# Optimization experiments

Measured on AMD Instinct MI355X. Metric: run time of the kernel, lower is better.

## Reference

```python
import jax, jax.numpy as jnp
import numpy as np

DIRECTIONS = [(0, 0), (1, 0), (-1, 0), (0, 1), (0, -1)]  # (dx, dy)
BN_EPS = 1e-5


def shift2d(x, directions=DIRECTIONS):
    # x: (B, C, H, W). Split channels into G groups, roll each spatially,
    # zero out the wrapped-around border (zero_pad mode), then concat.
    C = x.shape[1]
    G = len(directions)
    base = C // G
    sizes = [base] * (G - 1) + [C - base * (G - 1)]
    starts = np.concatenate([[0], np.cumsum(sizes)])
    out = []
    for i, (dx, dy) in enumerate(directions):
        chunk = x[:, starts[i]:starts[i + 1]]
        if dx == 0 and dy == 0:
            out.append(chunk)
            continue
        y = jnp.roll(chunk, shift=(dy, dx), axis=(-2, -1))
        if dy > 0:
            y = y.at[..., :dy, :].set(0.0)
        elif dy < 0:
            y = y.at[..., dy:, :].set(0.0)
        if dx > 0:
            y = y.at[..., :, :dx].set(0.0)
        elif dx < 0:
            y = y.at[..., :, dx:].set(0.0)
        out.append(y)
    return jnp.concatenate(out, axis=1)


def setup_inputs() -> dict:
    key = jax.random.key(0)
    k1, k2, k3, k4 = jax.random.split(key, 4)
    B, Cin, Cout, H, W = 32, 256, 256, 56, 56
    x = jax.random.normal(k1, (B, Cin, H, W), dtype=jnp.float32)
    pw_w = jax.random.normal(k2, (Cout, Cin), dtype=jnp.float32) * (1.0 / np.sqrt(Cin))
    gamma = jnp.ones((Cout,), dtype=jnp.float32)
    beta = jnp.zeros((Cout,), dtype=jnp.float32)
    running_mean = jax.random.normal(k3, (Cout,), dtype=jnp.float32) * 0.1
    running_var = jax.random.uniform(k4, (Cout,), dtype=jnp.float32, minval=0.5, maxval=1.5)
    return {"x": x, "pw_w": pw_w, "gamma": gamma, "beta": beta,
            "running_mean": running_mean, "running_var": running_var}


def reference(x, pw_w, gamma, beta, running_mean, running_var):
    # Shift (parameter-free spatial mixing)
    y = shift2d(x)
    # stride=1 -> down is Identity
    # 1x1 conv (no bias): pointwise channel mixing
    y = jnp.einsum('bchw,oc->bohw', y, pw_w)
    # BatchNorm2d (inference form with running stats) + ReLU
    inv = gamma * jax.lax.rsqrt(running_var + BN_EPS)
    y = y * inv[None, :, None, None] + (beta - running_mean * inv)[None, :, None, None]
    return jax.nn.relu(y)
```

## Files before the change

### kernel.cpp

```cpp
#include <hip/hip_runtime.h>

#define H_ 56
#define W_ 56
#define HW_ 3136
#define CIN_ 256
#define COUT_ 256

typedef __attribute__((ext_vector_type(8))) short short8;
typedef __attribute__((ext_vector_type(4))) float f32x4;

__device__ unsigned short g_wbf[COUT_ * CIN_];

__device__ __forceinline__ unsigned short f2bf(float f) {
  union { float f; unsigned int i; } v; v.f = f;
  unsigned int b = v.i + (0x7fffu + ((v.i >> 16) & 1u));
  return (unsigned short)(b >> 16);
}

__device__ __forceinline__ void gload_lds16(const unsigned short* g, unsigned short* l) {
  __builtin_amdgcn_global_load_lds(
      (const __attribute__((address_space(1))) unsigned int*)g,
      (__attribute__((address_space(3))) unsigned int*)l, 16, 0, 0);
}

__global__ __launch_bounds__(256)
void prep_weights(const float* __restrict__ wgt) {
  int idx = blockIdx.x * 256 + threadIdx.x;
  int bm  = idx >> 15;
  int kt  = (idx >> 13) & 3;
  int e   = idx & 8191;
  int m   = e >> 6;
  int u   = (e >> 3) & 7;
  int j   = e & 7;
  int o   = bm * 128 + m;
  int k   = kt * 64 + (((u ^ (m & 7)) << 3) | j);
  g_wbf[idx] = f2bf(wgt[o * CIN_ + k]);
}

__global__ __launch_bounds__(256, 3)
void shiftconv_gemm(const float* __restrict__ x,
                    const float* __restrict__ gamma,
                    const float* __restrict__ beta,
                    const float* __restrict__ rmean,
                    const float* __restrict__ rvar,
                    float* __restrict__ out)
{
  __shared__ unsigned short Alds[2][128 * 64];
  __shared__ unsigned short Blds[2][64 * 64];
  __shared__ float bnp[256];

  const int t = threadIdx.x;
  const int orig = blockIdx.x;
  const int wgid = (orig & 7) * 392 + (orig >> 3);
  const int bm   = wgid & 1;
  const int bn   = wgid >> 1;

  const int lane = t & 63;
  const int wv   = t >> 6;
  const int wm   = wv >> 1;
  const int wn   = wv & 1;
  const int quad = lane >> 4;
  const int l15  = lane & 15;

  if (t < 128) {
    int o = bm * 128 + t;
    float inv = gamma[o] * rsqrtf(rvar[o] + 1e-5f);
    bnp[2 * t]     = inv;
    bnp[2 * t + 1] = beta[o] - rmean[o] * inv;
  }

  const int nl    = t & 63;
  const int kg    = __builtin_amdgcn_readfirstlane(t >> 6);
  const int kg16  = kg << 4;
  const int nglob = bn * 64 + nl;
  const int bidx  = nglob / HW_;
  const int rem   = nglob - bidx * HW_;
  const int hh    = rem / W_;
  const int ww    = rem - hh * W_;
  const float* __restrict__ px = x + (size_t)bidx * CIN_ * HW_ + hh * W_ + ww;
  const bool mL = (ww >= 1);
  const bool mR = (ww <= W_ - 2);
  const bool mU = (hh >= 1);
  const bool mD = (hh <= H_ - 2);
  const int  h7 = nl & 7;
  unsigned short* const bpA = &Blds[0][nl * 64];
  unsigned short* const bpB = &Blds[1][nl * 64];

  const unsigned short* wsrc = g_wbf + bm * 32768 + t * 8;

  f32x4 acc[4][2];
  #pragma unroll
  for (int i = 0; i < 4; ++i)
    #pragma unroll
    for (int j = 0; j < 2; ++j)
      acc[i][j] = (f32x4){0.f, 0.f, 0.f, 0.f};

  float fv[16];

  auto loadB = [&](int kt4) {
    #pragma unroll
    for (int j = 0; j < 16; ++j) {
      int c = kt4 * 64 + kg16 + j;
      int r = (c >= 51) + (c >= 102) + (c >= 153) + (c >= 204);
      int off = (r == 1) ? -1 : (r == 2) ? 1 : (r == 3) ? -W_ :
                (r == 4) ? W_ : 0;
      bool mm = (r == 0) | ((r == 1) & mL) | ((r == 2) & mR) |
                ((r == 3) & mU) | ((r == 4) & mD);
      const float* p = px + (size_t)c * HW_;
      float v = p[mm ? off : 0];
      fv[j] = mm ? v : 0.f;
    }
  };
  auto writeB = [&](unsigned short* bp) {
    union { short8 v; unsigned short s[8]; } pa, pb;
    #pragma unroll
    for (int j = 0; j < 8; ++j) { pa.s[j] = f2bf(fv[j]); pb.s[j] = f2bf(fv[8 + j]); }
    int s0 = kg * 2;
    *(short8*)(bp + (((s0    ) ^ h7) << 3)) = pa.v;
    *(short8*)(bp + (((s0 | 1) ^ h7) << 3)) = pb.v;
  };
  auto stageA = [&](int bsel, int kt4) {
    const unsigned short* g = wsrc + kt4 * 8192;
    unsigned short* l = &Alds[bsel][t * 8];
    gload_lds16(g,        l);
    gload_lds16(g + 2048, l + 2048);
    gload_lds16(g + 4096, l + 4096);
    gload_lds16(g + 6144, l + 6144);
  };

  stageA(0, 0);
  loadB(0);
  writeB(bpA);
  __syncthreads();

  int buf = 0;

  for (int kt = 0; kt < 4; ++kt) {
    if (kt < 3) {
      stageA(buf ^ 1, kt + 1);
      loadB(kt + 1);
    }

    #pragma unroll
    for (int ks = 0; ks < 2; ++ks) {
      const int sA = ks * 4 + quad;
      short8 af[4], bfr[2];
      #pragma unroll
      for (int f = 0; f < 4; ++f) {
        int ml = wm * 64 + f * 16 + l15;
        af[f] = *(const short8*)(&Alds[buf][ml * 64 + ((sA ^ (ml & 7)) << 3)]);
      }
      #pragma unroll
      for (int g2 = 0; g2 < 2; ++g2) {
        int nl2 = wn * 32 + g2 * 16 + l15;
        bfr[g2] = *(const short8*)(&Blds[buf][nl2 * 64 + ((sA ^ (nl2 & 7)) << 3)]);
      }
      #pragma unroll
      for (int mf = 0; mf < 4; ++mf)
        #pragma unroll
        for (int nf = 0; nf < 2; ++nf)
          acc[mf][nf] = __builtin_amdgcn_mfma_f32_16x16x32_bf16(
              af[mf], bfr[nf], acc[mf][nf], 0, 0, 0);
    }

    if (kt < 3)
      writeB((buf ^ 1) ? bpB : bpA);

    __syncthreads();
    buf ^= 1;
  }

  size_t nbase[2];
  #pragma unroll
  for (int nf = 0; nf < 2; ++nf) {
    int ng  = bn * 64 + wn * 32 + nf * 16 + l15;
    int b2  = ng / HW_;
    int hw2 = ng - b2 * HW_;
    nbase[nf] = (size_t)b2 * COUT_ * HW_ + hw2;
  }
  #pragma unroll
  for (int mf = 0; mf < 4; ++mf) {
    int mloc = wm * 64 + mf * 16 + quad * 4;
    float inv[4], add[4];
    #pragma unroll
    for (int r = 0; r < 4; ++r) {
      inv[r] = bnp[2 * (mloc + r)];
      add[r] = bnp[2 * (mloc + r) + 1];
    }
    size_t obase = (size_t)(bm * 128 + mloc) * HW_;
    #pragma unroll
    for (int nf = 0; nf < 2; ++nf) {
      #pragma unroll
      for (int r = 0; r < 4; ++r) {
        float v = fmaf(acc[mf][nf][r], inv[r], add[r]);
        out[nbase[nf] + obase + (size_t)r * HW_] = fmaxf(v, 0.0f);
      }
    }
  }
}

extern "C" void kernel_launch(void* const* d_in, const int* in_sizes, int n_in,
                              void* d_out, int out_size, void* d_ws, size_t ws_size,
                              hipStream_t stream) {
  const float* x     = (const float*)d_in[0];
  const float* wgt   = (const float*)d_in[1];
  const float* gamma = (const float*)d_in[2];
  const float* beta  = (const float*)d_in[3];
  const float* rmean = (const float*)d_in[4];
  const float* rvar  = (const float*)d_in[5];
  float* out = (float*)d_out;

  prep_weights<<<dim3(256), dim3(256), 0, stream>>>(wgt);
  shiftconv_gemm<<<dim3(3136), dim3(256), 0, stream>>>(x, gamma, beta, rmean, rvar, out);
}
```

Baseline: 243.1 us.

## Load weight MFMA fragments directly from global memory, drop A LDS staging

Reorders the prepared bf16 weights into per-wave MFMA fragment order so each wave reads its A operands straight from global/L2 instead of staging them through LDS. This removes the A shared-memory buffers, which cuts LDS use and allows raising the occupancy hint to 4 blocks per CU. The B conversion also switches to packed v_cvt_pk_bf16_f32 instructions. The trade-off is that weight fragments are now fetched from cache by every wave without LDS reuse, adding global-load latency inside the MFMA loop.

```diff
diff --git a/kernel.cpp b/kernel.cpp
--- a/kernel.cpp
+++ b/kernel.cpp
@@ -17,27 +17,21 @@
   return (unsigned short)(b >> 16);
 }
 
-__device__ __forceinline__ void gload_lds16(const unsigned short* g, unsigned short* l) {
-  __builtin_amdgcn_global_load_lds(
-      (const __attribute__((address_space(1))) unsigned int*)g,
-      (__attribute__((address_space(3))) unsigned int*)l, 16, 0, 0);
+__global__ __launch_bounds__(256)
+void prep_weights(const float* __restrict__ wgt) {
+  int idx  = blockIdx.x * 256 + threadIdx.x;
+  int j    = idx & 7;
+  int lane = (idx >> 3) & 63;
+  int f    = (idx >> 9) & 3;
+  int ks   = (idx >> 11) & 7;
+  int wm   = (idx >> 14) & 1;
+  int bm   = idx >> 15;
+  int m = bm * 128 + wm * 64 + f * 16 + (lane & 15);
+  int k = ks * 32 + (lane >> 4) * 8 + j;
+  g_wbf[idx] = f2bf(wgt[m * CIN_ + k]);
 }
 
-__global__ __launch_bounds__(256)
-void prep_weights(const float* __restrict__ wgt) {
-  int idx = blockIdx.x * 256 + threadIdx.x;
-  int bm  = idx >> 15;
-  int kt  = (idx >> 13) & 3;
-  int e   = idx & 8191;
-  int m   = e >> 6;
-  int u   = (e >> 3) & 7;
-  int j   = e & 7;
-  int o   = bm * 128 + m;
-  int k   = kt * 64 + (((u ^ (m & 7)) << 3) | j);
-  g_wbf[idx] = f2bf(wgt[o * CIN_ + k]);
-}
-
-__global__ __launch_bounds__(256, 3)
+__global__ __launch_bounds__(256, 4)
 void shiftconv_gemm(const float* __restrict__ x,
                     const float* __restrict__ gamma,
                     const float* __restrict__ beta,
@@ -45,7 +39,6 @@
                     const float* __restrict__ rvar,
                     float* __restrict__ out)
 {
-  __shared__ unsigned short Alds[2][128 * 64];
   __shared__ unsigned short Blds[2][64 * 64];
   __shared__ float bnp[256];
 
@@ -86,7 +79,7 @@
   unsigned short* const bpA = &Blds[0][nl * 64];
   unsigned short* const bpB = &Blds[1][nl * 64];
 
-  const unsigned short* wsrc = g_wbf + bm * 32768 + t * 8;
+  const unsigned short* afrag = g_wbf + (size_t)(bm * 2 + wm) * 16384 + lane * 8;
 
   f32x4 acc[4][2];
   #pragma unroll
@@ -112,23 +105,17 @@
     }
   };
   auto writeB = [&](unsigned short* bp) {
-    union { short8 v; unsigned short s[8]; } pa, pb;
+    unsigned int da[4], db[4];
     #pragma unroll
-    for (int j = 0; j < 8; ++j) { pa.s[j] = f2bf(fv[j]); pb.s[j] = f2bf(fv[8 + j]); }
+    for (int j = 0; j < 4; ++j) {
+      asm("v_cvt_pk_bf16_f32 %0, %1, %2" : "=v"(da[j]) : "v"(fv[2*j]),     "v"(fv[2*j+1]));
+      asm("v_cvt_pk_bf16_f32 %0, %1, %2" : "=v"(db[j]) : "v"(fv[8+2*j]),   "v"(fv[8+2*j+1]));
+    }
     int s0 = kg * 2;
-    *(short8*)(bp + (((s0    ) ^ h7) << 3)) = pa.v;
-    *(short8*)(bp + (((s0 | 1) ^ h7) << 3)) = pb.v;
-  };
-  auto stageA = [&](int bsel, int kt4) {
-    const unsigned short* g = wsrc + kt4 * 8192;
-    unsigned short* l = &Alds[bsel][t * 8];
-    gload_lds16(g,        l);
-    gload_lds16(g + 2048, l + 2048);
-    gload_lds16(g + 4096, l + 4096);
-    gload_lds16(g + 6144, l + 6144);
+    *(uint4*)(bp + (((s0    ) ^ h7) << 3)) = make_uint4(da[0], da[1], da[2], da[3]);
+    *(uint4*)(bp + (((s0 | 1) ^ h7) << 3)) = make_uint4(db[0], db[1], db[2], db[3]);
   };
 
-  stageA(0, 0);
   loadB(0);
   writeB(bpA);
   __syncthreads();
@@ -136,20 +123,16 @@
   int buf = 0;
 
   for (int kt = 0; kt < 4; ++kt) {
-    if (kt < 3) {
-      stageA(buf ^ 1, kt + 1);
-      loadB(kt + 1);
-    }
+    if (kt < 3) loadB(kt + 1);
 
     #pragma unroll
-    for (int ks = 0; ks < 2; ++ks) {
-      const int sA = ks * 4 + quad;
+    for (int ks2 = 0; ks2 < 2; ++ks2) {
+      const int kss = kt * 2 + ks2;
+      const int sA  = ks2 * 4 + quad;
       short8 af[4], bfr[2];
       #pragma unroll
-      for (int f = 0; f < 4; ++f) {
-        int ml = wm * 64 + f * 16 + l15;
-        af[f] = *(const short8*)(&Alds[buf][ml * 64 + ((sA ^ (ml & 7)) << 3)]);
-      }
+      for (int f = 0; f < 4; ++f)
+        af[f] = *(const short8*)(afrag + kss * 2048 + f * 512);
       #pragma unroll
       for (int g2 = 0; g2 < 2; ++g2) {
         int nl2 = wn * 32 + g2 * 16 + l15;
```

New measurement: 225.8 us. -7.1%, faster.
